# Kernel tuning notes

Hardware: AMD Instinct MI355X
Metric: run time of the kernel (lower is better)

## Reference

```python
import jax, jax.numpy as jnp
import numpy as np
from functools import partial

B = 256          # batch_size (== hidden_dim, required by the module's broadcasting)
T = 512          # seq_length
H = 256          # hidden_dim == dim_out
E = 6            # emb_dim
V = 10           # num_input_digits
C = 10           # num_classes


def _kaiming(key, shape):
    fan_in = shape[1]
    return jax.random.normal(key, shape, dtype=jnp.float32) * np.sqrt(2.0 / fan_in)


def setup_inputs() -> dict:
    key = jax.random.key(0)
    ks = jax.random.split(key, 12)
    inp = {
        "x": jax.random.randint(ks[0], (B, T), 0, V),
        "emb": jax.random.normal(ks[1], (V, E), dtype=jnp.float32),
        "Wxg": _kaiming(ks[2], (H, E)), "Whg": _kaiming(ks[3], (H, H)), "bg": jnp.zeros((H,), jnp.float32),
        "Wxi": _kaiming(ks[4], (H, E)), "Whi": _kaiming(ks[5], (H, H)), "bi": jnp.zeros((H,), jnp.float32),
        "Wxf": _kaiming(ks[6], (H, E)), "Whf": _kaiming(ks[7], (H, H)), "bf": jnp.zeros((H,), jnp.float32),
        "Wxo": _kaiming(ks[8], (H, E)), "Who": _kaiming(ks[9], (H, H)), "bo": jnp.zeros((H,), jnp.float32),
        "Wp": _kaiming(ks[10], (C, H)), "bp": jnp.zeros((C,), jnp.float32),
    }
    return inp


def reference(x, emb, Wxg, Whg, bg, Wxi, Whi, bi, Wxf, Whf, bf, Wxo, Who, bo, Wp, bp):
    # x: (B, T) int -> embed -> (B, T, E)
    xe = emb[x]
    # time-major (T, E, B): each step uses x_t.T as in the torch code
    xt_seq = jnp.transpose(xe, (1, 2, 0))

    h0 = jnp.zeros((H, B), jnp.float32)  # h lives as (H, B) per original math
    c0 = jnp.zeros((H, B), jnp.float32)

    def step(carry, xTt):  # xTt: (E, B)
        h, c = carry
        # NOTE: bias (H,) broadcasts over the trailing batch axis (H==B), faithful
        # to the original torch broadcasting.
        g = jnp.tanh(Wxg @ xTt + Whg @ h + bg)
        i = jax.nn.sigmoid(Wxi @ xTt + Whi @ h + bi)
        f = jax.nn.sigmoid(Wxf @ xTt + Whf @ h + bf)
        o = jax.nn.sigmoid(Wxo @ xTt + Who @ h + bo)
        c = g * i + c * f
        h = jnp.tanh(c) * o
        return (h, c), None

    (h, c), _ = jax.lax.scan(step, (h0, c0), xt_seq)
    return (Wp @ h).T + bp  # (B, C)
```

## Files before the change

kernel.cpp:

```cpp
#include <hip/hip_runtime.h>
#include <hip/hip_bf16.h>


typedef __attribute__((ext_vector_type(4))) int   int4v;
typedef __attribute__((ext_vector_type(4))) float float4v;

#define MFMA_I8(a, b, c) __builtin_amdgcn_mfma_i32_16x16x64_i8(a, b, c, 0, 0, 0)

#define K_TANH (-2.8853900817779268f)
#define K_SIG  (-1.4426950408889634f)

#define HSTRIDE 320

__device__ __forceinline__ short f2b(float f) {
    __hip_bfloat16 b = __float2bfloat16(f); return *(short*)&b;
}
__device__ __forceinline__ float b2f(short s) {
    union { unsigned int u; float f; } v; v.u = ((unsigned int)(unsigned short)s) << 16; return v.f;
}
__device__ __forceinline__ float fexp2(float x) {
#if __has_builtin(__builtin_amdgcn_exp2f)
    return __builtin_amdgcn_exp2f(x);
#else
    return __expf(x * 0.6931471805599453f);
#endif
}
__device__ __forceinline__ float frcp(float x) { return __builtin_amdgcn_rcpf(x); }

__global__ __attribute__((amdgpu_flat_work_group_size(1024, 1024), amdgpu_waves_per_eu(4, 4)))
void lstm_i8(
    const int* __restrict__ x,
    const float* __restrict__ emb,
    const float* __restrict__ Wxg, const float* __restrict__ Whg, const float* __restrict__ bg,
    const float* __restrict__ Wxi, const float* __restrict__ Whi, const float* __restrict__ bi,
    const float* __restrict__ Wxf, const float* __restrict__ Whf, const float* __restrict__ bff,
    const float* __restrict__ Wxo, const float* __restrict__ Who, const float* __restrict__ bo,
    const float* __restrict__ Wp, const float* __restrict__ bp,
    float* __restrict__ out)
{
    const int tid = threadIdx.x, bid = blockIdx.x;
    const int c0 = bid * 2;
    const int w = tid >> 6, lane = tid & 63;
    const int l = lane & 15, q = lane >> 4;
    const int col = l & 1;
    const int si  = (l >> 1) & 3;
    const int dup = (l >> 3) & 1;
    const int rw  = 16 * w;
    const int row = rw + 4 * q + si;

    __shared__ __align__(16) unsigned int hbuf[2][2 * HSTRIDE / 4];
    __shared__ __align__(16) short hfin[2 * 264];
    __shared__ unsigned char xdig2[512 * 2];
    __shared__ __align__(16) float tblT[10 * 1024];
    __shared__ float scaleL[4 * 256];

    const float* WxT[4] = {Wxg, Wxi, Wxf, Wxo};
    const float* WhT[4] = {Whg, Whi, Whf, Who};

    if (tid < 2 * HSTRIDE / 4) hbuf[0][tid] = 0u;
    if (tid < 1024)
        xdig2[tid] = (unsigned char)x[(c0 + (tid & 1)) * 512 + (tid >> 1)];

    for (int i = tid; i < 2560; i += 1024) {
        int d = i >> 8, r = i & 255;
        float4v v;
        #pragma unroll
        for (int g = 0; g < 4; g++) {
            float s = 0.f;
            #pragma unroll
            for (int e = 0; e < 6; e++) s += WxT[g][r * 6 + e] * emb[d * 6 + e];
            v[g] = s * (g == 0 ? K_TANH : K_SIG);
        }
        *(float4v*)&tblT[d * 1024 + r * 4] = v;
    }

    int4v wa[4][4];
    #pragma unroll
    for (int g = 0; g < 4; g++) {
        const float* Wr = WhT[g] + (rw + l) * 256 + q * 16;
        float mx = 0.f;
        #pragma unroll
        for (int kt = 0; kt < 4; kt++)
            #pragma unroll
            for (int c4 = 0; c4 < 4; c4++) {
                float4v v = *(const float4v*)(Wr + kt * 64 + c4 * 4);
                #pragma unroll
                for (int j = 0; j < 4; j++) mx = fmaxf(mx, fabsf(v[j]));
            }
        mx = fmaxf(mx, __shfl_xor(mx, 16));
        mx = fmaxf(mx, __shfl_xor(mx, 32));
        mx = fmaxf(mx, 1e-20f);
        if (q == 0) scaleL[g * 256 + rw + l] = mx;
        float qs = 127.f / mx;
        #pragma unroll
        for (int kt = 0; kt < 4; kt++) {
            int4v f;
            #pragma unroll
            for (int dw = 0; dw < 4; dw++) {
                float4v v = *(const float4v*)(Wr + kt * 64 + dw * 4);
                int word = 0;
                #pragma unroll
                for (int byt = 0; byt < 4; byt++) {
                    int z = (int)rintf(v[byt] * qs);
                    word |= (z & 255) << (8 * byt);
                }
                f[dw] = word;
            }
            wa[g][kt] = f;
        }
    }

    __syncthreads();

    float dscl[4];
    #pragma unroll
    for (int g = 0; g < 4; g++) {
        float kk = (g == 0 ? K_TANH : K_SIG) * (1.f / 16129.f);
        dscl[g] = scaleL[g * 256 + row] * kk;
    }
    float bSc[4];
    bSc[0] = bg[c0 + col] * K_TANH; bSc[1] = bi[c0 + col] * K_SIG;
    bSc[2] = bff[c0 + col] * K_SIG; bSc[3] = bo[c0 + col] * K_SIG;

    const bool bi1 = (si & 1) != 0;
    const bool bi2 = (si & 2) != 0;
    const float* tprow = tblT + row * 4;
    const int hoff = col * HSTRIDE + row;

    float cs = 0.f, hl = 0.f;

    for (int t = 0; t < 512; t++) {
        const int p = t & 1;
        const char* hbase = (const char*)hbuf[p] + col * HSTRIDE + q * 16;

        int4v acc[4];
        #pragma unroll
        for (int g = 0; g < 4; g++) acc[g] = (int4v){0, 0, 0, 0};

        int dg = xdig2[t * 2 + col];
        float4v tb = *(const float4v*)(tprow + dg * 1024);

        #pragma unroll
        for (int kt = 0; kt < 4; kt++) {
            int4v hf = *(const int4v*)(hbase + kt * 64);
            #pragma unroll
            for (int g = 0; g < 4; g++)
                acc[g] = MFMA_I8(wa[g][kt], hf, acc[g]);
        }

        int av[4];
        #pragma unroll
        for (int g = 0; g < 4; g++) {
            int s0 = bi1 ? acc[g][1] : acc[g][0];
            int s1 = bi1 ? acc[g][3] : acc[g][2];
            av[g]  = bi2 ? s1 : s0;
        }
        {
            float pg = fmaf((float)av[0], dscl[0], tb[0] + bSc[0]);
            float pi = fmaf((float)av[1], dscl[1], tb[1] + bSc[1]);
            float pf = fmaf((float)av[2], dscl[2], tb[2] + bSc[2]);
            float po = fmaf((float)av[3], dscl[3], tb[3] + bSc[3]);
            float Eg = fexp2(pg), Ei = fexp2(pi), Ef = fexp2(pf), Eo = fexp2(po);
            float t1 = (1.f - Eg) * frcp((1.f + Eg) * (1.f + Ei));
            float c  = fmaf(cs, frcp(1.f + Ef), t1);
            cs = c;
            float Ec = fexp2(K_TANH * c);
            float hh = (1.f - Ec) * frcp((1.f + Ec) * (1.f + Eo));
            hl = hh;
            if (dup == 0)
                *((char*)hbuf[1 - p] + hoff) = (char)((int)rintf(hh * 127.f));
        }
        __syncthreads();
    }

    if (dup == 0) hfin[col * 264 + row] = f2b(hl);
    __syncthreads();

    if (tid < 20) {
        int pc = tid / 10, cls = tid - pc * 10;
        const short* hcol = &hfin[pc * 264];
        const float* wrow = Wp + cls * 256;
        float s = 0.f;
        #pragma unroll 8
        for (int k = 0; k < 256; k++) s += b2f(hcol[k]) * wrow[k];
        out[(c0 + pc) * 10 + cls] = s + bp[cls];
    }
}

extern "C" void kernel_launch(void* const* d_in, const int* in_sizes, int n_in,
                              void* d_out, int out_size, void* d_ws, size_t ws_size,
                              hipStream_t stream) {
    const int*   x   = (const int*)d_in[0];
    const float* emb = (const float*)d_in[1];
    const float* Wxg = (const float*)d_in[2];
    const float* Whg = (const float*)d_in[3];
    const float* bg  = (const float*)d_in[4];
    const float* Wxi = (const float*)d_in[5];
    const float* Whi = (const float*)d_in[6];
    const float* bi  = (const float*)d_in[7];
    const float* Wxf = (const float*)d_in[8];
    const float* Whf = (const float*)d_in[9];
    const float* bff = (const float*)d_in[10];
    const float* Wxo = (const float*)d_in[11];
    const float* Who = (const float*)d_in[12];
    const float* bo  = (const float*)d_in[13];
    const float* Wp  = (const float*)d_in[14];
    const float* bp  = (const float*)d_in[15];

    hipLaunchKernelGGL(lstm_i8, dim3(128), dim3(1024), 0, stream,
                       x, emb, Wxg, Whg, bg, Wxi, Whi, bi, Wxf, Whf, bff,
                       Wxo, Who, bo, Wp, bp, (float*)d_out);
}
```

Before: 573.6 us.

## Fold bias into per-column input table and split MFMA accumulator chains

```diff
diff --git a/kernel.cpp b/kernel.cpp
--- a/kernel.cpp
+++ b/kernel.cpp
@@ -51,27 +51,30 @@
     __shared__ __align__(16) unsigned int hbuf[2][2 * HSTRIDE / 4];
     __shared__ __align__(16) short hfin[2 * 264];
     __shared__ unsigned char xdig2[512 * 2];
-    __shared__ __align__(16) float tblT[10 * 1024];
+    __shared__ __align__(16) float tblC[2 * 10 * 1024];
     __shared__ float scaleL[4 * 256];
 
     const float* WxT[4] = {Wxg, Wxi, Wxf, Wxo};
     const float* WhT[4] = {Whg, Whi, Whf, Who};
+    const float* bT[4]  = {bg, bi, bff, bo};
 
     if (tid < 2 * HSTRIDE / 4) hbuf[0][tid] = 0u;
     if (tid < 1024)
         xdig2[tid] = (unsigned char)x[(c0 + (tid & 1)) * 512 + (tid >> 1)];
 
-    for (int i = tid; i < 2560; i += 1024) {
-        int d = i >> 8, r = i & 255;
+    for (int i = tid; i < 5120; i += 1024) {
+        int cc  = i / 2560;
+        int rem = i - cc * 2560;
+        int d = rem >> 8, r = rem & 255;
         float4v v;
         #pragma unroll
         for (int g = 0; g < 4; g++) {
             float s = 0.f;
             #pragma unroll
             for (int e = 0; e < 6; e++) s += WxT[g][r * 6 + e] * emb[d * 6 + e];
-            v[g] = s * (g == 0 ? K_TANH : K_SIG);
+            v[g] = (s + bT[g][c0 + cc]) * (g == 0 ? K_TANH : K_SIG);
         }
-        *(float4v*)&tblT[d * 1024 + r * 4] = v;
+        *(float4v*)&tblC[cc * 10240 + d * 1024 + r * 4] = v;
     }
 
     int4v wa[4][4];
@@ -118,13 +121,10 @@
         float kk = (g == 0 ? K_TANH : K_SIG) * (1.f / 16129.f);
         dscl[g] = scaleL[g * 256 + row] * kk;
     }
-    float bSc[4];
-    bSc[0] = bg[c0 + col] * K_TANH; bSc[1] = bi[c0 + col] * K_SIG;
-    bSc[2] = bff[c0 + col] * K_SIG; bSc[3] = bo[c0 + col] * K_SIG;
 
     const bool bi1 = (si & 1) != 0;
     const bool bi2 = (si & 2) != 0;
-    const float* tprow = tblT + row * 4;
+    const float* tprow = tblC + col * 10240 + row * 4;
     const int hoff = col * HSTRIDE + row;
 
     float cs = 0.f, hl = 0.f;
@@ -133,36 +133,43 @@
         const int p = t & 1;
         const char* hbase = (const char*)hbuf[p] + col * HSTRIDE + q * 16;
 
-        int4v acc[4];
-        #pragma unroll
-        for (int g = 0; g < 4; g++) acc[g] = (int4v){0, 0, 0, 0};
-
         int dg = xdig2[t * 2 + col];
         float4v tb = *(const float4v*)(tprow + dg * 1024);
 
-        #pragma unroll
-        for (int kt = 0; kt < 4; kt++) {
-            int4v hf = *(const int4v*)(hbase + kt * 64);
-            #pragma unroll
-            for (int g = 0; g < 4; g++)
-                acc[g] = MFMA_I8(wa[g][kt], hf, acc[g]);
-        }
-
-        int av[4];
-        #pragma unroll
-        for (int g = 0; g < 4; g++) {
-            int s0 = bi1 ? acc[g][1] : acc[g][0];
-            int s1 = bi1 ? acc[g][3] : acc[g][2];
-            av[g]  = bi2 ? s1 : s0;
-        }
+        int4v a0e = {0,0,0,0}, a0o = {0,0,0,0};
+        int4v a1e = {0,0,0,0}, a1o = {0,0,0,0};
+        int4v a2  = {0,0,0,0}, a3  = {0,0,0,0};
+        int4v hf0 = *(const int4v*)(hbase + 0 * 64);
+        int4v hf1 = *(const int4v*)(hbase + 1 * 64);
+        int4v hf2 = *(const int4v*)(hbase + 2 * 64);
+        int4v hf3 = *(const int4v*)(hbase + 3 * 64);
+        a0e = MFMA_I8(wa[0][0], hf0, a0e); a0o = MFMA_I8(wa[0][1], hf1, a0o);
+        a1e = MFMA_I8(wa[1][0], hf0, a1e); a1o = MFMA_I8(wa[1][1], hf1, a1o);
+        a2  = MFMA_I8(wa[2][0], hf0, a2);  a2  = MFMA_I8(wa[2][1], hf1, a2);
+        a3  = MFMA_I8(wa[3][0], hf0, a3);  a3  = MFMA_I8(wa[3][1], hf1, a3);
+        a0e = MFMA_I8(wa[0][2], hf2, a0e); a0o = MFMA_I8(wa[0][3], hf3, a0o);
+        a1e = MFMA_I8(wa[1][2], hf2, a1e); a1o = MFMA_I8(wa[1][3], hf3, a1o);
+        a2  = MFMA_I8(wa[2][2], hf2, a2);  a2  = MFMA_I8(wa[2][3], hf3, a2);
+        a3  = MFMA_I8(wa[3][2], hf2, a3);  a3  = MFMA_I8(wa[3][3], hf3, a3);
+        int4v acc0, acc1;
+        #pragma unroll
+        for (int i = 0; i < 4; i++) { acc0[i] = a0e[i] + a0o[i]; acc1[i] = a1e[i] + a1o[i]; }
+
+        int av0, av1, av2, av3;
+        { int s0 = bi1 ? acc0[1] : acc0[0]; int s1 = bi1 ? acc0[3] : acc0[2]; av0 = bi2 ? s1 : s0; }
+        { int s0 = bi1 ? acc1[1] : acc1[0]; int s1 = bi1 ? acc1[3] : acc1[2]; av1 = bi2 ? s1 : s0; }
+        { int s0 = bi1 ? a2[1]   : a2[0];   int s1 = bi1 ? a2[3]   : a2[2];   av2 = bi2 ? s1 : s0; }
+        { int s0 = bi1 ? a3[1]   : a3[0];   int s1 = bi1 ? a3[3]   : a3[2];   av3 = bi2 ? s1 : s0; }
         {
-            float pg = fmaf((float)av[0], dscl[0], tb[0] + bSc[0]);
-            float pi = fmaf((float)av[1], dscl[1], tb[1] + bSc[1]);
-            float pf = fmaf((float)av[2], dscl[2], tb[2] + bSc[2]);
-            float po = fmaf((float)av[3], dscl[3], tb[3] + bSc[3]);
+            float pg = fmaf((float)av0, dscl[0], tb[0]);
+            float pi = fmaf((float)av1, dscl[1], tb[1]);
+            float pf = fmaf((float)av2, dscl[2], tb[2]);
+            float po = fmaf((float)av3, dscl[3], tb[3]);
             float Eg = fexp2(pg), Ei = fexp2(pi), Ef = fexp2(pf), Eo = fexp2(po);
-            float t1 = (1.f - Eg) * frcp((1.f + Eg) * (1.f + Ei));
-            float c  = fmaf(cs, frcp(1.f + Ef), t1);
+            float m1  = (1.f + Eg) * (1.f + Ei);
+            float fp1 = 1.f + Ef;
+            float num = fmaf(cs, m1, (1.f - Eg) * fp1);
+            float c   = num * frcp(m1 * fp1);
             cs = c;
             float Ec = fexp2(K_TANH * c);
             float hh = (1.f - Ec) * frcp((1.f + Ec) * (1.f + Eo));
```

After: 555.9 us. 3.1% less time.
